# Kernel optimization log

Measured on AMD Instinct MI355X. Metric: run time of the kernel, lower is better.

## Reference

```python
import jax, jax.numpy as jnp
import numpy as np

I = 1024
H = 1024
B = 4096
EPS = 1e-5

def layer_norm(x, gamma, beta):
    mu = jnp.mean(x, axis=-1, keepdims=True)
    var = jnp.var(x, axis=-1, keepdims=True)
    return (x - mu) * jax.lax.rsqrt(var + EPS) * gamma + beta

def setup_inputs() -> dict:
    key = jax.random.key(0)
    ks = jax.random.split(key, 5)
    return {
        "input": jax.random.normal(ks[0], (B, I), dtype=jnp.float32),
        "hx": jax.random.normal(ks[1], (B, H), dtype=jnp.float32),
        "cx": jax.random.normal(ks[2], (B, H), dtype=jnp.float32),
        "weight_ih": jax.random.normal(ks[3], (4 * H, I), dtype=jnp.float32),
        "weight_hh": jax.random.normal(ks[4], (4 * H, H), dtype=jnp.float32),
        "gamma_i": jnp.ones((4 * H,), jnp.float32),
        "beta_i": jnp.zeros((4 * H,), jnp.float32),
        "gamma_h": jnp.ones((4 * H,), jnp.float32),
        "beta_h": jnp.zeros((4 * H,), jnp.float32),
        "gamma_c": jnp.ones((H,), jnp.float32),
        "beta_c": jnp.zeros((H,), jnp.float32),
    }

def reference(input, hx, cx, weight_ih, weight_hh,
              gamma_i, beta_i, gamma_h, beta_h, gamma_c, beta_c):
    # igates: [B, 4H]
    igates = layer_norm(jnp.dot(input, weight_ih.T), gamma_i, beta_i)
    hgates = layer_norm(jnp.dot(hx, weight_hh.T), gamma_h, beta_h)
    gates = igates + hgates
    ingate, forgetgate, cellgate, outgate = jnp.split(gates, 4, axis=1)
    ingate = jax.nn.sigmoid(ingate)
    forgetgate = jax.nn.sigmoid(forgetgate)
    cellgate = jnp.tanh(cellgate)
    outgate = jax.nn.sigmoid(outgate)
    cy = layer_norm(forgetgate * cx + ingate * cellgate, gamma_c, beta_c)
    hy = outgate * jnp.tanh(cy)
    return (hy, hy, cy)
```

## Files before the change

### kernel.cpp

```cpp
#include <hip/hip_runtime.h>

#define EPS 1e-5f

typedef unsigned short u16;
typedef __attribute__((ext_vector_type(8))) __bf16 bf16x8;
typedef __attribute__((ext_vector_type(4))) float f32x4;
typedef __attribute__((ext_vector_type(8))) unsigned short ushort8;

__device__ inline float bf2f(u16 h) {
  union { unsigned u; float f; } x; x.u = ((unsigned)h) << 16; return x.f;
}
__device__ inline u16 f2bf(float f) {
  union { float f; unsigned u; } x; x.f = f;
  unsigned r = x.u + 0x7fffu + ((x.u >> 16) & 1u);
  return (u16)(r >> 16);
}
__device__ inline float sigmoidf(float x) { return 1.0f / (1.0f + __expf(-x)); }

__global__ __launch_bounds__(256) void cast4_f32_bf16(
    const float* __restrict__ s0, const float* __restrict__ s1,
    const float* __restrict__ s2, const float* __restrict__ s3,
    u16* __restrict__ d0, u16* __restrict__ d1,
    u16* __restrict__ d2, u16* __restrict__ d3, int n)
{
  const float* s = (blockIdx.y == 0) ? s0 : (blockIdx.y == 1) ? s1 : (blockIdx.y == 2) ? s2 : s3;
  u16*         d = (blockIdx.y == 0) ? d0 : (blockIdx.y == 1) ? d1 : (blockIdx.y == 2) ? d2 : d3;
  int i = (blockIdx.x * 256 + threadIdx.x) * 8;
  if (i >= n) return;
  float4 a = *(const float4*)(s + i);
  float4 b = *(const float4*)(s + i + 4);
  ushort8 o;
  o[0] = f2bf(a.x); o[1] = f2bf(a.y); o[2] = f2bf(a.z); o[3] = f2bf(a.w);
  o[4] = f2bf(b.x); o[5] = f2bf(b.y); o[6] = f2bf(b.z); o[7] = f2bf(b.w);
  *(ushort8*)(d + i) = o;
}

#define MFMA_ __builtin_amdgcn_mfma_f32_16x16x32_bf16

#define STAGE_A(nx, k0) { _Pragma("unroll") for (int i_ = 0; i_ < 4; ++i_) \
  __builtin_amdgcn_global_load_lds( \
      (const __attribute__((address_space(1))) void*)(gA + (size_t)(i_ * 64) * K + (k0)), \
      (__attribute__((address_space(3))) void*)(&sA[nx][(i_ * 512 + (w << 6)) * 8]), 16, 0, 0); }
#define STAGE_B(nx, k0) { _Pragma("unroll") for (int i_ = 0; i_ < 4; ++i_) \
  __builtin_amdgcn_global_load_lds( \
      (const __attribute__((address_space(1))) void*)(gB + (size_t)(i_ * 64) * K + (k0)), \
      (__attribute__((address_space(3))) void*)(&sB[nx][(i_ * 512 + (w << 6)) * 8]), 16, 0, 0); }

#define LDA(mi, sl) (*(const bf16x8*)&sa[(arow + (mi) * 16) * 64 + (sl)])
#define LDB(ni, sl) (*(const bf16x8*)&sb[(brow + (ni) * 16) * 64 + (sl)])

#define PHASE(m0, sl, RB) { \
  bf16x8 a0 = LDA(m0 + 0, sl), a1 = LDA(m0 + 1, sl), a2 = LDA(m0 + 2, sl), a3 = LDA(m0 + 3, sl); \
  if (RB) { q0 = LDB(0, sl); q1 = LDB(1, sl); q2 = LDB(2, sl); q3 = LDB(3, sl); } \
  __builtin_amdgcn_s_barrier(); \
  __builtin_amdgcn_s_setprio(1); \
  acc[m0 + 0][0] = MFMA_(a0, q0, acc[m0 + 0][0], 0, 0, 0); \
  acc[m0 + 0][1] = MFMA_(a0, q1, acc[m0 + 0][1], 0, 0, 0); \
  acc[m0 + 0][2] = MFMA_(a0, q2, acc[m0 + 0][2], 0, 0, 0); \
  acc[m0 + 0][3] = MFMA_(a0, q3, acc[m0 + 0][3], 0, 0, 0); \
  acc[m0 + 1][0] = MFMA_(a1, q0, acc[m0 + 1][0], 0, 0, 0); \
  acc[m0 + 1][1] = MFMA_(a1, q1, acc[m0 + 1][1], 0, 0, 0); \
  acc[m0 + 1][2] = MFMA_(a1, q2, acc[m0 + 1][2], 0, 0, 0); \
  acc[m0 + 1][3] = MFMA_(a1, q3, acc[m0 + 1][3], 0, 0, 0); \
  acc[m0 + 2][0] = MFMA_(a2, q0, acc[m0 + 2][0], 0, 0, 0); \
  acc[m0 + 2][1] = MFMA_(a2, q1, acc[m0 + 2][1], 0, 0, 0); \
  acc[m0 + 2][2] = MFMA_(a2, q2, acc[m0 + 2][2], 0, 0, 0); \
  acc[m0 + 2][3] = MFMA_(a2, q3, acc[m0 + 2][3], 0, 0, 0); \
  acc[m0 + 3][0] = MFMA_(a3, q0, acc[m0 + 3][0], 0, 0, 0); \
  acc[m0 + 3][1] = MFMA_(a3, q1, acc[m0 + 3][1], 0, 0, 0); \
  acc[m0 + 3][2] = MFMA_(a3, q2, acc[m0 + 3][2], 0, 0, 0); \
  acc[m0 + 3][3] = MFMA_(a3, q3, acc[m0 + 3][3], 0, 0, 0); \
  __builtin_amdgcn_s_setprio(0); }

__global__ __launch_bounds__(512, 2) void gemm256_dual(
    const u16* __restrict__ A0, const u16* __restrict__ W0, u16* __restrict__ C0,
    const u16* __restrict__ A1, const u16* __restrict__ W1, u16* __restrict__ C1)
{
  constexpr int K = 1024, N = 4096, NT = 16;

  __shared__ __attribute__((aligned(16))) u16 sA[2][256 * 64];
  __shared__ __attribute__((aligned(16))) u16 sB[2][256 * 64];

  const int bid = blockIdx.x;
  const u16* A  = (bid < 256) ? A0 : A1;
  const u16* Wm = (bid < 256) ? W0 : W1;
  u16*       C  = (bid < 256) ? C0 : C1;
  const int b2 = bid & 255;
  const int bm = (b2 >> 4) << 8;
  const int bn = (b2 & 15) << 8;

  const int tid = threadIdx.x;
  const int l  = tid & 63;
  const int w  = tid >> 6;
  const int wr = w >> 2;
  const int wc = w & 3;

  const int rb   = tid >> 3;
  const int slot = (tid & 7) ^ (rb & 7);
  const u16* gA = A  + (size_t)(bm + rb) * K + slot * 8;
  const u16* gB = Wm + (size_t)(bn + rb) * K + slot * 8;

  const int arow = wr * 128 + (l & 15);
  const int brow = wc * 64 + (l & 15);
  const int sl0 = (((l >> 4) + 0) ^ (l & 7)) * 8;
  const int sl1 = (((l >> 4) + 4) ^ (l & 7)) * 8;

  f32x4 acc[8][4];
#pragma unroll
  for (int i = 0; i < 8; ++i)
#pragma unroll
    for (int j = 0; j < 4; ++j) acc[i][j] = (f32x4){0.f, 0.f, 0.f, 0.f};

  STAGE_A(0, 0)
  STAGE_B(0, 0)
  __syncthreads();

  for (int t = 0; t < NT; ++t) {
    const int cur = t & 1, nxt = cur ^ 1;
    const int kn = (t + 1) << 6;
    const u16* sa = sA[cur];
    const u16* sb = sB[cur];
    bf16x8 q0, q1, q2, q3;

    if (t < NT - 1) STAGE_A(nxt, kn)
    PHASE(0, sl0, 1)
    __builtin_amdgcn_s_barrier();
    if (t < NT - 1) STAGE_B(nxt, kn)
    PHASE(4, sl0, 0)
    __builtin_amdgcn_s_barrier();
    PHASE(0, sl1, 1)
    __builtin_amdgcn_s_barrier();
    PHASE(4, sl1, 0)
    __syncthreads();
  }

  const int ccol = bn + wc * 64 + (l & 15);
  const int crow = bm + wr * 128 + (l >> 4) * 4;
#pragma unroll
  for (int mi = 0; mi < 8; ++mi) {
#pragma unroll
    for (int ni = 0; ni < 4; ++ni) {
      int col = ccol + ni * 16;
#pragma unroll
      for (int r = 0; r < 4; ++r) {
        int row = crow + mi * 16 + r;
        C[(size_t)row * N + col] = f2bf(acc[mi][ni][r]);
      }
    }
  }
}

__global__ __launch_bounds__(256) void lstm_epilogue(
    const u16* __restrict__ ig, const u16* __restrict__ hg,
    const float* __restrict__ cx,
    const float* __restrict__ gi, const float* __restrict__ bi,
    const float* __restrict__ gh, const float* __restrict__ bh,
    const float* __restrict__ gc, const float* __restrict__ bc,
    float* __restrict__ out)
{
  const int b = blockIdx.x;
  const int t = threadIdx.x;
  const u16* igr = ig + (size_t)b * 4096;
  const u16* hgr = hg + (size_t)b * 4096;

  __shared__ float redbuf[16];

  float iv[16], hv[16];
  float s_i = 0.f, q_i = 0.f, s_h = 0.f, q_h = 0.f;
#pragma unroll
  for (int i = 0; i < 16; ++i) {
    float a = bf2f(igr[t + 256 * i]);
    float c = bf2f(hgr[t + 256 * i]);
    iv[i] = a; hv[i] = c;
    s_i += a; q_i += a * a; s_h += c; q_h += c * c;
  }
#pragma unroll
  for (int off = 32; off > 0; off >>= 1) {
    s_i += __shfl_xor(s_i, off);
    q_i += __shfl_xor(q_i, off);
    s_h += __shfl_xor(s_h, off);
    q_h += __shfl_xor(q_h, off);
  }
  {
    int wv = t >> 6;
    if ((t & 63) == 0) {
      redbuf[wv] = s_i; redbuf[wv + 4] = q_i;
      redbuf[wv + 8] = s_h; redbuf[wv + 12] = q_h;
    }
    __syncthreads();
    s_i = redbuf[0] + redbuf[1] + redbuf[2] + redbuf[3];
    q_i = redbuf[4] + redbuf[5] + redbuf[6] + redbuf[7];
    s_h = redbuf[8] + redbuf[9] + redbuf[10] + redbuf[11];
    q_h = redbuf[12] + redbuf[13] + redbuf[14] + redbuf[15];
    __syncthreads();
  }
  const float inv4096 = 1.0f / 4096.0f;
  float mu_i = s_i * inv4096;
  float rs_i = rsqrtf(q_i * inv4096 - mu_i * mu_i + EPS);
  float mu_h = s_h * inv4096;
  float rs_h = rsqrtf(q_h * inv4096 - mu_h * mu_h + EPS);

  float c_pre[4], og[4];
  float s_c = 0.f, q_c = 0.f;
#pragma unroll
  for (int i = 0; i < 4; ++i) {
    int h = t + 256 * i;
    float g_in = ((iv[i]      - mu_i) * rs_i * gi[h]        + bi[h]) +
                 ((hv[i]      - mu_h) * rs_h * gh[h]        + bh[h]);
    float g_fg = ((iv[i + 4]  - mu_i) * rs_i * gi[h + 1024] + bi[h + 1024]) +
                 ((hv[i + 4]  - mu_h) * rs_h * gh[h + 1024] + bh[h + 1024]);
    float g_cl = ((iv[i + 8]  - mu_i) * rs_i * gi[h + 2048] + bi[h + 2048]) +
                 ((hv[i + 8]  - mu_h) * rs_h * gh[h + 2048] + bh[h + 2048]);
    float g_og = ((iv[i + 12] - mu_i) * rs_i * gi[h + 3072] + bi[h + 3072]) +
                 ((hv[i + 12] - mu_h) * rs_h * gh[h + 3072] + bh[h + 3072]);
    float in_s = sigmoidf(g_in);
    float fg_s = sigmoidf(g_fg);
    float cl_t = tanhf(g_cl);
    og[i] = sigmoidf(g_og);
    c_pre[i] = fg_s * cx[(size_t)b * 1024 + h] + in_s * cl_t;
    s_c += c_pre[i]; q_c += c_pre[i] * c_pre[i];
  }
#pragma unroll
  for (int off = 32; off > 0; off >>= 1) {
    s_c += __shfl_xor(s_c, off);
    q_c += __shfl_xor(q_c, off);
  }
  {
    int wv = t >> 6;
    if ((t & 63) == 0) { redbuf[wv] = s_c; redbuf[wv + 4] = q_c; }
    __syncthreads();
    s_c = redbuf[0] + redbuf[1] + redbuf[2] + redbuf[3];
    q_c = redbuf[4] + redbuf[5] + redbuf[6] + redbuf[7];
  }
  const float inv1024 = 1.0f / 1024.0f;
  float mu_c = s_c * inv1024;
  float rs_c = rsqrtf(q_c * inv1024 - mu_c * mu_c + EPS);

  const size_t BH = (size_t)4096 * 1024;
#pragma unroll
  for (int i = 0; i < 4; ++i) {
    int h = t + 256 * i;
    float cy = (c_pre[i] - mu_c) * rs_c * gc[h] + bc[h];
    float hy = og[i] * tanhf(cy);
    size_t o = (size_t)b * 1024 + h;
    out[o] = hy;
    out[BH + o] = hy;
    out[2 * BH + o] = cy;
  }
}

extern "C" void kernel_launch(void* const* d_in, const int* in_sizes, int n_in,
                              void* d_out, int out_size, void* d_ws, size_t ws_size,
                              hipStream_t stream) {
  const float* input = (const float*)d_in[0];
  const float* hx    = (const float*)d_in[1];
  const float* cx    = (const float*)d_in[2];
  const float* wih   = (const float*)d_in[3];
  const float* whh   = (const float*)d_in[4];
  const float* gi    = (const float*)d_in[5];
  const float* bi    = (const float*)d_in[6];
  const float* gh    = (const float*)d_in[7];
  const float* bh    = (const float*)d_in[8];
  const float* gc    = (const float*)d_in[9];
  const float* bc    = (const float*)d_in[10];
  float* out = (float*)d_out;

  char* wsp = (char*)d_ws;
  u16* a_bf  = (u16*)(wsp);
  u16* h_bf  = (u16*)(wsp + ((size_t)8  << 20));
  u16* wi_bf = (u16*)(wsp + ((size_t)16 << 20));
  u16* wh_bf = (u16*)(wsp + ((size_t)24 << 20));
  u16* ig_bf = (u16*)(wsp + ((size_t)32 << 20));
  u16* hg_bf = (u16*)(wsp + ((size_t)64 << 20));

  const int nper = 4096 * 1024;
  dim3 cgrid(nper / 8 / 256, 4);
  cast4_f32_bf16<<<cgrid, 256, 0, stream>>>(input, hx, wih, whh,
                                            a_bf, h_bf, wi_bf, wh_bf, nper);

  gemm256_dual<<<512, 512, 0, stream>>>(a_bf, wi_bf, ig_bf,
                                        h_bf, wh_bf, hg_bf);

  lstm_epilogue<<<4096, 256, 0, stream>>>(ig_bf, hg_bf, cx,
                                          gi, bi, gh, bh, gc, bc, out);
}
```

Baseline: 134.0 us.

## Use partial vmcnt waits instead of full syncthreads and remap block IDs

Replaces the end-of-iteration __syncthreads with a targeted s_waitcnt vmcnt(4) plus barrier at the start of the next iteration. The loads for the next A tile can then stay in flight while the previous B tile is consumed. The last K tile is peeled into its own block. Block IDs are also remapped so consecutive hardware blocks are spread across the two GEMMs and tile positions, which is likely meant to balance XCD/L2 usage. The risk is ordering: the handwritten waitcnt counts must match the number of outstanding global_load_lds ops, and the LDS write-after-read protection for the buffer being overwritten now relies on those counts.

```diff
diff --git a/kernel.cpp b/kernel.cpp
--- a/kernel.cpp
+++ b/kernel.cpp
@@ -49,10 +49,7 @@
 #define LDA(mi, sl) (*(const bf16x8*)&sa[(arow + (mi) * 16) * 64 + (sl)])
 #define LDB(ni, sl) (*(const bf16x8*)&sb[(brow + (ni) * 16) * 64 + (sl)])
 
-#define PHASE(m0, sl, RB) { \
-  bf16x8 a0 = LDA(m0 + 0, sl), a1 = LDA(m0 + 1, sl), a2 = LDA(m0 + 2, sl), a3 = LDA(m0 + 3, sl); \
-  if (RB) { q0 = LDB(0, sl); q1 = LDB(1, sl); q2 = LDB(2, sl); q3 = LDB(3, sl); } \
-  __builtin_amdgcn_s_barrier(); \
+#define MFMA16(m0) \
   __builtin_amdgcn_s_setprio(1); \
   acc[m0 + 0][0] = MFMA_(a0, q0, acc[m0 + 0][0], 0, 0, 0); \
   acc[m0 + 0][1] = MFMA_(a0, q1, acc[m0 + 0][1], 0, 0, 0); \
@@ -70,7 +67,18 @@
   acc[m0 + 3][1] = MFMA_(a3, q1, acc[m0 + 3][1], 0, 0, 0); \
   acc[m0 + 3][2] = MFMA_(a3, q2, acc[m0 + 3][2], 0, 0, 0); \
   acc[m0 + 3][3] = MFMA_(a3, q3, acc[m0 + 3][3], 0, 0, 0); \
-  __builtin_amdgcn_s_setprio(0); }
+  __builtin_amdgcn_s_setprio(0);
+
+#define PHASE(m0, sl, RB) { \
+  bf16x8 a0 = LDA(m0 + 0, sl), a1 = LDA(m0 + 1, sl), a2 = LDA(m0 + 2, sl), a3 = LDA(m0 + 3, sl); \
+  if (RB) { q0 = LDB(0, sl); q1 = LDB(1, sl); q2 = LDB(2, sl); q3 = LDB(3, sl); } \
+  __builtin_amdgcn_s_barrier(); \
+  MFMA16(m0) }
+
+#define PHASE_NOBAR(m0, sl, RB) { \
+  bf16x8 a0 = LDA(m0 + 0, sl), a1 = LDA(m0 + 1, sl), a2 = LDA(m0 + 2, sl), a3 = LDA(m0 + 3, sl); \
+  if (RB) { q0 = LDB(0, sl); q1 = LDB(1, sl); q2 = LDB(2, sl); q3 = LDB(3, sl); } \
+  MFMA16(m0) }
 
 __global__ __launch_bounds__(512, 2) void gemm256_dual(
     const u16* __restrict__ A0, const u16* __restrict__ W0, u16* __restrict__ C0,
@@ -81,7 +89,9 @@
   __shared__ __attribute__((aligned(16))) u16 sA[2][256 * 64];
   __shared__ __attribute__((aligned(16))) u16 sB[2][256 * 64];
 
-  const int bid = blockIdx.x;
+  const int b0  = blockIdx.x;
+  const int bid = (b0 & 7) * 64 + (b0 >> 3);
+
   const u16* A  = (bid < 256) ? A0 : A1;
   const u16* Wm = (bid < 256) ? W0 : W1;
   u16*       C  = (bid < 256) ? C0 : C1;
@@ -113,25 +123,40 @@
 
   STAGE_A(0, 0)
   STAGE_B(0, 0)
-  __syncthreads();
-
-  for (int t = 0; t < NT; ++t) {
+
+  for (int t = 0; t < NT - 1; ++t) {
     const int cur = t & 1, nxt = cur ^ 1;
     const int kn = (t + 1) << 6;
     const u16* sa = sA[cur];
     const u16* sb = sB[cur];
     bf16x8 q0, q1, q2, q3;
 
-    if (t < NT - 1) STAGE_A(nxt, kn)
-    PHASE(0, sl0, 1)
-    __builtin_amdgcn_s_barrier();
-    if (t < NT - 1) STAGE_B(nxt, kn)
+    STAGE_A(nxt, kn)
+    asm volatile("s_waitcnt vmcnt(4)" ::: "memory");
+    __builtin_amdgcn_s_barrier();
+    PHASE_NOBAR(0, sl0, 1)
+    __builtin_amdgcn_s_barrier();
+    STAGE_B(nxt, kn)
     PHASE(4, sl0, 0)
     __builtin_amdgcn_s_barrier();
     PHASE(0, sl1, 1)
     __builtin_amdgcn_s_barrier();
     PHASE(4, sl1, 0)
-    __syncthreads();
+  }
+
+  {
+    const u16* sa = sA[(NT - 1) & 1];
+    const u16* sb = sB[(NT - 1) & 1];
+    bf16x8 q0, q1, q2, q3;
+    asm volatile("s_waitcnt vmcnt(0)" ::: "memory");
+    __builtin_amdgcn_s_barrier();
+    PHASE_NOBAR(0, sl0, 1)
+    __builtin_amdgcn_s_barrier();
+    PHASE(4, sl0, 0)
+    __builtin_amdgcn_s_barrier();
+    PHASE(0, sl1, 1)
+    __builtin_amdgcn_s_barrier();
+    PHASE(4, sl1, 0)
   }
 
   const int ccol = bn + wc * 64 + (l & 15);
```

Result: faster. 125.2 us (-6.6%).

## Rework GEMM k-loop with vmcnt-gated staging, split B prefetch and XCD block remap

Applied to the files above, without the earlier changes.

Restructures the dual GEMM main loop so each k-tile reads both B k-halves from LDS once and iterates over A row pairs. Staging of the next A and B tiles is interleaved between the MFMA phases, with split B loads. Full __syncthreads are replaced by an explicit s_waitcnt vmcnt plus s_barrier, and the last iteration is peeled. Block IDs are also remapped so consecutive tiles land on the same XCD, for better L2 reuse. This aims to hide global-to-LDS latency and cut LDS reloads of B, at the cost of more live registers and tighter correctness reliance on the hand-placed wait counts.

```diff
diff --git a/kernel.cpp b/kernel.cpp
--- a/kernel.cpp
+++ b/kernel.cpp
@@ -37,40 +37,48 @@
 
 #define MFMA_ __builtin_amdgcn_mfma_f32_16x16x32_bf16
 
-#define STAGE_A(nx, k0) { _Pragma("unroll") for (int i_ = 0; i_ < 4; ++i_) \
+#define STAGE_A(nx, kt) { _Pragma("unroll") for (int i_ = 0; i_ < 4; ++i_) \
   __builtin_amdgcn_global_load_lds( \
-      (const __attribute__((address_space(1))) void*)(gA + (size_t)(i_ * 64) * K + (k0)), \
+      (const __attribute__((address_space(1))) void*)(gA + (size_t)(i_ * 64) * K + (kt)), \
       (__attribute__((address_space(3))) void*)(&sA[nx][(i_ * 512 + (w << 6)) * 8]), 16, 0, 0); }
-#define STAGE_B(nx, k0) { _Pragma("unroll") for (int i_ = 0; i_ < 4; ++i_) \
+
+#define STAGE_B_H(nx, kt, h) { _Pragma("unroll") for (int i_ = 2*(h); i_ < 2*(h)+2; ++i_) \
   __builtin_amdgcn_global_load_lds( \
-      (const __attribute__((address_space(1))) void*)(gB + (size_t)(i_ * 64) * K + (k0)), \
+      (const __attribute__((address_space(1))) void*)(gB + (size_t)(i_ * 64) * K + (kt)), \
       (__attribute__((address_space(3))) void*)(&sB[nx][(i_ * 512 + (w << 6)) * 8]), 16, 0, 0); }
 
-#define LDA(mi, sl) (*(const bf16x8*)&sa[(arow + (mi) * 16) * 64 + (sl)])
-#define LDB(ni, sl) (*(const bf16x8*)&sb[(brow + (ni) * 16) * 64 + (sl)])
-
-#define PHASE(m0, sl, RB) { \
-  bf16x8 a0 = LDA(m0 + 0, sl), a1 = LDA(m0 + 1, sl), a2 = LDA(m0 + 2, sl), a3 = LDA(m0 + 3, sl); \
-  if (RB) { q0 = LDB(0, sl); q1 = LDB(1, sl); q2 = LDB(2, sl); q3 = LDB(3, sl); } \
+#define LDA_(mi, sl) (*(const bf16x8*)&sa[(arow + (mi) * 16) * 64 + (sl)])
+#define LDB_(ni, sl) (*(const bf16x8*)&sb[(brow + (ni) * 16) * 64 + (sl)])
+
+#define PH_TOPQ(m0) \
+  q00 = LDB_(0, sl0); q01 = LDB_(1, sl0); q02 = LDB_(2, sl0); q03 = LDB_(3, sl0); \
+  q10 = LDB_(0, sl1); q11 = LDB_(1, sl1); q12 = LDB_(2, sl1); q13 = LDB_(3, sl1); \
+  x0 = LDA_(m0, sl0); x1 = LDA_(m0, sl1); x2 = LDA_(m0 + 1, sl0); x3 = LDA_(m0 + 1, sl1);
+
+#define PH_TOPA(m0) \
+  x0 = LDA_(m0, sl0); x1 = LDA_(m0, sl1); x2 = LDA_(m0 + 1, sl0); x3 = LDA_(m0 + 1, sl1);
+
+#define PH_BOT(m0) \
   __builtin_amdgcn_s_barrier(); \
   __builtin_amdgcn_s_setprio(1); \
-  acc[m0 + 0][0] = MFMA_(a0, q0, acc[m0 + 0][0], 0, 0, 0); \
-  acc[m0 + 0][1] = MFMA_(a0, q1, acc[m0 + 0][1], 0, 0, 0); \
-  acc[m0 + 0][2] = MFMA_(a0, q2, acc[m0 + 0][2], 0, 0, 0); \
-  acc[m0 + 0][3] = MFMA_(a0, q3, acc[m0 + 0][3], 0, 0, 0); \
-  acc[m0 + 1][0] = MFMA_(a1, q0, acc[m0 + 1][0], 0, 0, 0); \
-  acc[m0 + 1][1] = MFMA_(a1, q1, acc[m0 + 1][1], 0, 0, 0); \
-  acc[m0 + 1][2] = MFMA_(a1, q2, acc[m0 + 1][2], 0, 0, 0); \
-  acc[m0 + 1][3] = MFMA_(a1, q3, acc[m0 + 1][3], 0, 0, 0); \
-  acc[m0 + 2][0] = MFMA_(a2, q0, acc[m0 + 2][0], 0, 0, 0); \
-  acc[m0 + 2][1] = MFMA_(a2, q1, acc[m0 + 2][1], 0, 0, 0); \
-  acc[m0 + 2][2] = MFMA_(a2, q2, acc[m0 + 2][2], 0, 0, 0); \
-  acc[m0 + 2][3] = MFMA_(a2, q3, acc[m0 + 2][3], 0, 0, 0); \
-  acc[m0 + 3][0] = MFMA_(a3, q0, acc[m0 + 3][0], 0, 0, 0); \
-  acc[m0 + 3][1] = MFMA_(a3, q1, acc[m0 + 3][1], 0, 0, 0); \
-  acc[m0 + 3][2] = MFMA_(a3, q2, acc[m0 + 3][2], 0, 0, 0); \
-  acc[m0 + 3][3] = MFMA_(a3, q3, acc[m0 + 3][3], 0, 0, 0); \
-  __builtin_amdgcn_s_setprio(0); }
+  acc[m0 + 0][0] = MFMA_(x0, q00, acc[m0 + 0][0], 0, 0, 0); \
+  acc[m0 + 0][1] = MFMA_(x0, q01, acc[m0 + 0][1], 0, 0, 0); \
+  acc[m0 + 0][2] = MFMA_(x0, q02, acc[m0 + 0][2], 0, 0, 0); \
+  acc[m0 + 0][3] = MFMA_(x0, q03, acc[m0 + 0][3], 0, 0, 0); \
+  acc[m0 + 1][0] = MFMA_(x2, q00, acc[m0 + 1][0], 0, 0, 0); \
+  acc[m0 + 1][1] = MFMA_(x2, q01, acc[m0 + 1][1], 0, 0, 0); \
+  acc[m0 + 1][2] = MFMA_(x2, q02, acc[m0 + 1][2], 0, 0, 0); \
+  acc[m0 + 1][3] = MFMA_(x2, q03, acc[m0 + 1][3], 0, 0, 0); \
+  acc[m0 + 0][0] = MFMA_(x1, q10, acc[m0 + 0][0], 0, 0, 0); \
+  acc[m0 + 0][1] = MFMA_(x1, q11, acc[m0 + 0][1], 0, 0, 0); \
+  acc[m0 + 0][2] = MFMA_(x1, q12, acc[m0 + 0][2], 0, 0, 0); \
+  acc[m0 + 0][3] = MFMA_(x1, q13, acc[m0 + 0][3], 0, 0, 0); \
+  acc[m0 + 1][0] = MFMA_(x3, q10, acc[m0 + 1][0], 0, 0, 0); \
+  acc[m0 + 1][1] = MFMA_(x3, q11, acc[m0 + 1][1], 0, 0, 0); \
+  acc[m0 + 1][2] = MFMA_(x3, q12, acc[m0 + 1][2], 0, 0, 0); \
+  acc[m0 + 1][3] = MFMA_(x3, q13, acc[m0 + 1][3], 0, 0, 0); \
+  __builtin_amdgcn_s_setprio(0); \
+  __builtin_amdgcn_s_barrier();
 
 __global__ __launch_bounds__(512, 2) void gemm256_dual(
     const u16* __restrict__ A0, const u16* __restrict__ W0, u16* __restrict__ C0,
@@ -81,7 +89,9 @@
   __shared__ __attribute__((aligned(16))) u16 sA[2][256 * 64];
   __shared__ __attribute__((aligned(16))) u16 sB[2][256 * 64];
 
-  const int bid = blockIdx.x;
+  const int b0  = blockIdx.x;
+  const int bid = (b0 & 7) * 64 + (b0 >> 3);
+
   const u16* A  = (bid < 256) ? A0 : A1;
   const u16* Wm = (bid < 256) ? W0 : W1;
   u16*       C  = (bid < 256) ? C0 : C1;
@@ -112,26 +122,45 @@
     for (int j = 0; j < 4; ++j) acc[i][j] = (f32x4){0.f, 0.f, 0.f, 0.f};
 
   STAGE_A(0, 0)
-  STAGE_B(0, 0)
-  __syncthreads();
-
-  for (int t = 0; t < NT; ++t) {
+  STAGE_B_H(0, 0, 0)
+  STAGE_B_H(0, 0, 1)
+
+  for (int t = 0; t < NT - 1; ++t) {
     const int cur = t & 1, nxt = cur ^ 1;
     const int kn = (t + 1) << 6;
     const u16* sa = sA[cur];
     const u16* sb = sB[cur];
-    bf16x8 q0, q1, q2, q3;
-
-    if (t < NT - 1) STAGE_A(nxt, kn)
-    PHASE(0, sl0, 1)
+    bf16x8 q00, q01, q02, q03, q10, q11, q12, q13, x0, x1, x2, x3;
+
+    STAGE_A(nxt, kn)
+    asm volatile("s_waitcnt vmcnt(4)" ::: "memory");
     __builtin_amdgcn_s_barrier();
-    if (t < NT - 1) STAGE_B(nxt, kn)
-    PHASE(4, sl0, 0)
+    PH_TOPQ(0)
+    STAGE_B_H(nxt, kn, 0)
+    PH_BOT(0)
+    PH_TOPA(2)
+    STAGE_B_H(nxt, kn, 1)
+    PH_BOT(2)
+    PH_TOPA(4)
+    PH_BOT(4)
+    PH_TOPA(6)
+    PH_BOT(6)
+  }
+
+  {
+    const u16* sa = sA[(NT - 1) & 1];
+    const u16* sb = sB[(NT - 1) & 1];
+    bf16x8 q00, q01, q02, q03, q10, q11, q12, q13, x0, x1, x2, x3;
+    asm volatile("s_waitcnt vmcnt(0)" ::: "memory");
     __builtin_amdgcn_s_barrier();
-    PHASE(0, sl1, 1)
-    __builtin_amdgcn_s_barrier();
-    PHASE(4, sl1, 0)
-    __syncthreads();
+    PH_TOPQ(0)
+    PH_BOT(0)
+    PH_TOPA(2)
+    PH_BOT(2)
+    PH_TOPA(4)
+    PH_BOT(4)
+    PH_TOPA(6)
+    PH_BOT(6)
   }
 
   const int ccol = bn + wc * 64 + (l & 15);
```

Result: faster. 125.0 us (-6.7%).

## Split K-tiles into halves with deeper prefetch pipeline and block swizzle

Applied to the files above, without the earlier changes.

Restructures the GEMM main loop so each 64-wide K tile is stored as two 32-wide halves in LDS. The half-buffer that was just consumed is refilled with data for tile t+2, which gives more global loads in flight, and explicit vmcnt/lgkmcnt waits replace the full __syncthreads. It also remaps block indices so that consecutive workgroups spread across XCDs, and it changes the LDS swizzle to a 4-slot XOR. The goal is to hide global-to-LDS latency better and improve L2 locality. The manual waitcnt counts are fragile: if they are wrong there is a data race, and more barriers could add stalls.

```diff
diff --git a/kernel.cpp b/kernel.cpp
--- a/kernel.cpp
+++ b/kernel.cpp
@@ -36,41 +36,56 @@
 }
 
 #define MFMA_ __builtin_amdgcn_mfma_f32_16x16x32_bf16
-
-#define STAGE_A(nx, k0) { _Pragma("unroll") for (int i_ = 0; i_ < 4; ++i_) \
-  __builtin_amdgcn_global_load_lds( \
-      (const __attribute__((address_space(1))) void*)(gA + (size_t)(i_ * 64) * K + (k0)), \
-      (__attribute__((address_space(3))) void*)(&sA[nx][(i_ * 512 + (w << 6)) * 8]), 16, 0, 0); }
-#define STAGE_B(nx, k0) { _Pragma("unroll") for (int i_ = 0; i_ < 4; ++i_) \
-  __builtin_amdgcn_global_load_lds( \
-      (const __attribute__((address_space(1))) void*)(gB + (size_t)(i_ * 64) * K + (k0)), \
-      (__attribute__((address_space(3))) void*)(&sB[nx][(i_ * 512 + (w << 6)) * 8]), 16, 0, 0); }
-
-#define LDA(mi, sl) (*(const bf16x8*)&sa[(arow + (mi) * 16) * 64 + (sl)])
-#define LDB(ni, sl) (*(const bf16x8*)&sb[(brow + (ni) * 16) * 64 + (sl)])
-
-#define PHASE(m0, sl, RB) { \
-  bf16x8 a0 = LDA(m0 + 0, sl), a1 = LDA(m0 + 1, sl), a2 = LDA(m0 + 2, sl), a3 = LDA(m0 + 3, sl); \
-  if (RB) { q0 = LDB(0, sl); q1 = LDB(1, sl); q2 = LDB(2, sl); q3 = LDB(3, sl); } \
-  __builtin_amdgcn_s_barrier(); \
+#define ASG __attribute__((address_space(1)))
+#define ASL __attribute__((address_space(3)))
+
+#define GLL(p, lds) __builtin_amdgcn_global_load_lds( \
+    (const ASG void*)(p), (ASL void*)(lds), 16, 0, 0);
+
+#define STG_A(buf, kh, tt) { \
+  GLL(gAs + (size_t)(tt) * 64 + (kh) * 32, &sA[buf][kh][tid * 8]) \
+  GLL(gAs + (size_t)128 * K + (size_t)(tt) * 64 + (kh) * 32, &sA[buf][kh][(512 + tid) * 8]) }
+#define STG_B(buf, kh, tt) { \
+  GLL(gBs + (size_t)(tt) * 64 + (kh) * 32, &sB[buf][kh][tid * 8]) \
+  GLL(gBs + (size_t)128 * K + (size_t)(tt) * 64 + (kh) * 32, &sB[buf][kh][(512 + tid) * 8]) }
+
+#define LDAf(buf, kh, mi) (*(const bf16x8*)&sA[buf][kh][(arow + (mi) * 16) * 32 + aslot])
+#define LDBf(buf, kh, ni) (*(const bf16x8*)&sB[buf][kh][(brow + (ni) * 16) * 32 + bslot])
+
+#define RD_AB(buf, kh, m0) \
+  a0 = LDAf(buf, kh, m0 + 0); a1 = LDAf(buf, kh, m0 + 1); \
+  a2 = LDAf(buf, kh, m0 + 2); a3 = LDAf(buf, kh, m0 + 3); \
+  b0 = LDBf(buf, kh, 0); b1 = LDBf(buf, kh, 1); \
+  b2 = LDBf(buf, kh, 2); b3 = LDBf(buf, kh, 3);
+
+#define RD_A(buf, kh, m0) \
+  a0 = LDAf(buf, kh, m0 + 0); a1 = LDAf(buf, kh, m0 + 1); \
+  a2 = LDAf(buf, kh, m0 + 2); a3 = LDAf(buf, kh, m0 + 3);
+
+#define BAR __builtin_amdgcn_s_barrier();
+#define LGKM0 { asm volatile("s_waitcnt lgkmcnt(0)" ::: "memory"); \
+                __builtin_amdgcn_sched_barrier(0); }
+#define VMW(n) asm volatile("s_waitcnt vmcnt(" #n ")" ::: "memory");
+
+#define PH_MFMA(m0) \
   __builtin_amdgcn_s_setprio(1); \
-  acc[m0 + 0][0] = MFMA_(a0, q0, acc[m0 + 0][0], 0, 0, 0); \
-  acc[m0 + 0][1] = MFMA_(a0, q1, acc[m0 + 0][1], 0, 0, 0); \
-  acc[m0 + 0][2] = MFMA_(a0, q2, acc[m0 + 0][2], 0, 0, 0); \
-  acc[m0 + 0][3] = MFMA_(a0, q3, acc[m0 + 0][3], 0, 0, 0); \
-  acc[m0 + 1][0] = MFMA_(a1, q0, acc[m0 + 1][0], 0, 0, 0); \
-  acc[m0 + 1][1] = MFMA_(a1, q1, acc[m0 + 1][1], 0, 0, 0); \
-  acc[m0 + 1][2] = MFMA_(a1, q2, acc[m0 + 1][2], 0, 0, 0); \
-  acc[m0 + 1][3] = MFMA_(a1, q3, acc[m0 + 1][3], 0, 0, 0); \
-  acc[m0 + 2][0] = MFMA_(a2, q0, acc[m0 + 2][0], 0, 0, 0); \
-  acc[m0 + 2][1] = MFMA_(a2, q1, acc[m0 + 2][1], 0, 0, 0); \
-  acc[m0 + 2][2] = MFMA_(a2, q2, acc[m0 + 2][2], 0, 0, 0); \
-  acc[m0 + 2][3] = MFMA_(a2, q3, acc[m0 + 2][3], 0, 0, 0); \
-  acc[m0 + 3][0] = MFMA_(a3, q0, acc[m0 + 3][0], 0, 0, 0); \
-  acc[m0 + 3][1] = MFMA_(a3, q1, acc[m0 + 3][1], 0, 0, 0); \
-  acc[m0 + 3][2] = MFMA_(a3, q2, acc[m0 + 3][2], 0, 0, 0); \
-  acc[m0 + 3][3] = MFMA_(a3, q3, acc[m0 + 3][3], 0, 0, 0); \
-  __builtin_amdgcn_s_setprio(0); }
+  acc[m0 + 0][0] = MFMA_(a0, b0, acc[m0 + 0][0], 0, 0, 0); \
+  acc[m0 + 0][1] = MFMA_(a0, b1, acc[m0 + 0][1], 0, 0, 0); \
+  acc[m0 + 0][2] = MFMA_(a0, b2, acc[m0 + 0][2], 0, 0, 0); \
+  acc[m0 + 0][3] = MFMA_(a0, b3, acc[m0 + 0][3], 0, 0, 0); \
+  acc[m0 + 1][0] = MFMA_(a1, b0, acc[m0 + 1][0], 0, 0, 0); \
+  acc[m0 + 1][1] = MFMA_(a1, b1, acc[m0 + 1][1], 0, 0, 0); \
+  acc[m0 + 1][2] = MFMA_(a1, b2, acc[m0 + 1][2], 0, 0, 0); \
+  acc[m0 + 1][3] = MFMA_(a1, b3, acc[m0 + 1][3], 0, 0, 0); \
+  acc[m0 + 2][0] = MFMA_(a2, b0, acc[m0 + 2][0], 0, 0, 0); \
+  acc[m0 + 2][1] = MFMA_(a2, b1, acc[m0 + 2][1], 0, 0, 0); \
+  acc[m0 + 2][2] = MFMA_(a2, b2, acc[m0 + 2][2], 0, 0, 0); \
+  acc[m0 + 2][3] = MFMA_(a2, b3, acc[m0 + 2][3], 0, 0, 0); \
+  acc[m0 + 3][0] = MFMA_(a3, b0, acc[m0 + 3][0], 0, 0, 0); \
+  acc[m0 + 3][1] = MFMA_(a3, b1, acc[m0 + 3][1], 0, 0, 0); \
+  acc[m0 + 3][2] = MFMA_(a3, b2, acc[m0 + 3][2], 0, 0, 0); \
+  acc[m0 + 3][3] = MFMA_(a3, b3, acc[m0 + 3][3], 0, 0, 0); \
+  __builtin_amdgcn_s_setprio(0);
 
 __global__ __launch_bounds__(512, 2) void gemm256_dual(
     const u16* __restrict__ A0, const u16* __restrict__ W0, u16* __restrict__ C0,
@@ -78,10 +93,12 @@
 {
   constexpr int K = 1024, N = 4096, NT = 16;
 
-  __shared__ __attribute__((aligned(16))) u16 sA[2][256 * 64];
-  __shared__ __attribute__((aligned(16))) u16 sB[2][256 * 64];
-
-  const int bid = blockIdx.x;
+  __shared__ __attribute__((aligned(16))) u16 sA[2][2][256 * 32];
+  __shared__ __attribute__((aligned(16))) u16 sB[2][2][256 * 32];
+
+  const int b0_ = blockIdx.x;
+  const int bid = (b0_ & 7) * 64 + (b0_ >> 3);
+
   const u16* A  = (bid < 256) ? A0 : A1;
   const u16* Wm = (bid < 256) ? W0 : W1;
   u16*       C  = (bid < 256) ? C0 : C1;
@@ -94,16 +111,17 @@
   const int w  = tid >> 6;
   const int wr = w >> 2;
   const int wc = w & 3;
-
-  const int rb   = tid >> 3;
-  const int slot = (tid & 7) ^ (rb & 7);
-  const u16* gA = A  + (size_t)(bm + rb) * K + slot * 8;
-  const u16* gB = Wm + (size_t)(bn + rb) * K + slot * 8;
+  (void)w;
+
+  const int srow  = tid >> 2;
+  const int sslot = (tid & 3) ^ (srow & 3);
+  const u16* gAs = A  + (size_t)(bm + srow) * K + sslot * 8;
+  const u16* gBs = Wm + (size_t)(bn + srow) * K + sslot * 8;
 
   const int arow = wr * 128 + (l & 15);
   const int brow = wc * 64 + (l & 15);
-  const int sl0 = (((l >> 4) + 0) ^ (l & 7)) * 8;
-  const int sl1 = (((l >> 4) + 4) ^ (l & 7)) * 8;
+  const int aslot = ((l >> 4) ^ (l & 3)) * 8;
+  const int bslot = aslot;
 
   f32x4 acc[8][4];
 #pragma unroll
@@ -111,27 +129,42 @@
 #pragma unroll
     for (int j = 0; j < 4; ++j) acc[i][j] = (f32x4){0.f, 0.f, 0.f, 0.f};
 
-  STAGE_A(0, 0)
-  STAGE_B(0, 0)
-  __syncthreads();
+  STG_A(0, 0, 0) STG_B(0, 0, 0)
+  STG_A(0, 1, 0) STG_B(0, 1, 0)
+  STG_A(1, 0, 1) STG_B(1, 0, 1)
+  VMW(8)
+  BAR
 
   for (int t = 0; t < NT; ++t) {
     const int cur = t & 1, nxt = cur ^ 1;
-    const int kn = (t + 1) << 6;
-    const u16* sa = sA[cur];
-    const u16* sb = sB[cur];
-    bf16x8 q0, q1, q2, q3;
-
-    if (t < NT - 1) STAGE_A(nxt, kn)
-    PHASE(0, sl0, 1)
-    __builtin_amdgcn_s_barrier();
-    if (t < NT - 1) STAGE_B(nxt, kn)
-    PHASE(4, sl0, 0)
-    __builtin_amdgcn_s_barrier();
-    PHASE(0, sl1, 1)
-    __builtin_amdgcn_s_barrier();
-    PHASE(4, sl1, 0)
-    __syncthreads();
+    bf16x8 a0, a1, a2, a3, b0, b1, b2, b3;
+
+    RD_AB(cur, 0, 0)
+    if (t < NT - 1) STG_A(nxt, 1, t + 1)
+    BAR LGKM0
+    PH_MFMA(0)
+    BAR
+
+    RD_A(cur, 0, 4)
+    if (t < NT - 1) STG_B(nxt, 1, t + 1)
+    BAR LGKM0
+    PH_MFMA(4)
+    if (t < NT - 1) { VMW(6) } else { VMW(0) }
+    BAR
+
+    RD_AB(cur, 1, 0)
+    if (t < NT - 2) STG_A(cur, 0, t + 2)
+    BAR LGKM0
+    PH_MFMA(0)
+    BAR
+
+    RD_A(cur, 1, 4)
+    if (t < NT - 2) STG_B(cur, 0, t + 2)
+    BAR LGKM0
+    PH_MFMA(4)
+    if (t < NT - 2) { VMW(6) }
+    else if (t == NT - 2) { VMW(4) }
+    BAR
   }
 
   const int ccol = bn + wc * 64 + (l & 15);
```

Result: faster. 128.3 us (-4.3%).
